# Kernel tuning notes

Hardware: AMD Instinct MI355X
Metric: run time of the kernel (lower is better)

The kernel has to match this reference:

```python
import jax, jax.numpy as jnp
import numpy as np

N = 6000          # num nodes (max_nodes)
E = 192000        # num edges
NTYPES = 100
NCLUST = 4        # hardcoded num_nodes=4 in diff_pool_net.__init__
OUT = 16
BN_EPS = 1e-5

PARAM_SHAPES = {
    'emb_w': (NTYPES, 64),
    # gnn1_pool: GNN(64, 64, 4, lin=True); DenseSAGEConv: lin_rel (no bias) + lin_root (bias)
    'pw1r': (64, 64), 'pw1l': (64, 64), 'pb1': (64,),
    'pw2r': (64, 64), 'pw2l': (64, 64), 'pb2': (64,),
    'pw3r': (NCLUST, 64), 'pw3l': (NCLUST, 64), 'pb3': (NCLUST,),
    'plin_w': (NCLUST, 2 * 64 + NCLUST), 'plin_b': (NCLUST,),
    # gnn1_embed: GNN(64, 64, 64, lin=False)
    'ew1r': (64, 64), 'ew1l': (64, 64), 'eb1': (64,),
    'ew2r': (64, 64), 'ew2l': (64, 64), 'eb2': (64,),
    'ew3r': (64, 64), 'ew3l': (64, 64), 'eb3': (64,),
    'lin1_w': (64, 192), 'lin1_b': (64,),
    'lin2_w': (OUT, 64), 'lin2_b': (OUT,),
    'embl_w': (32, 192), 'embl_b': (32,),
    'lin3_w': (OUT, 32 + OUT), 'lin3_b': (OUT,),
}


def _lin(x, w, b=None):
    y = x @ w.T
    return y if b is None else y + b


def _sage(x, adj, wr, wl, b):
    # DenseSAGEConv: mean-aggregate over dense adj, then lin_rel(agg) + lin_root(x)
    agg = jnp.matmul(adj, x)
    deg = jnp.clip(jnp.sum(adj, axis=-1, keepdims=True), 1.0, None)
    return _lin(agg / deg, wr) + _lin(x, wl, b)


def _bn(x):
    # training-mode BatchNorm1d with default gamma=1, beta=0 (biased variance)
    c = x.shape[-1]
    xf = x.reshape(-1, c)
    m = jnp.mean(xf, axis=0)
    v = jnp.var(xf, axis=0)
    return ((xf - m) * jax.lax.rsqrt(v + BN_EPS)).reshape(x.shape)


def _gnn(x, adj, wr1, wl1, b1, wr2, wl2, b2, wr3, wl3, b3, lw=None, lb=None):
    x1 = _bn(jax.nn.relu(_sage(x, adj, wr1, wl1, b1)))
    x2 = _bn(jax.nn.relu(_sage(x1, adj, wr2, wl2, b2)))
    x3 = _bn(jax.nn.relu(_sage(x2, adj, wr3, wl3, b3)))
    xc = jnp.concatenate([x1, x2, x3], axis=-1)
    if lw is not None:
        xc = jax.nn.relu(_lin(xc, lw, lb))
    return xc


def _forward(p, edge_index, node_types):
    # to_dense_adj: scatter-add edges into a dense [1, N, N] adjacency
    adj = jnp.zeros((N, N), jnp.float32).at[edge_index[0], edge_index[1]].add(1.0)[None]
    x = p['emb_w'][node_types][None]                      # [1, N, 64]
    s = _gnn(x, adj, p['pw1r'], p['pw1l'], p['pb1'],
             p['pw2r'], p['pw2l'], p['pb2'],
             p['pw3r'], p['pw3l'], p['pb3'],
             p['plin_w'], p['plin_b'])                    # [1, N, 4]
    xe = _gnn(x, adj, p['ew1r'], p['ew1l'], p['eb1'],
              p['ew2r'], p['ew2l'], p['eb2'],
              p['ew3r'], p['ew3l'], p['eb3'])             # [1, N, 192]
    x_embed = _lin(xe, p['embl_w'], p['embl_b'])          # [1, N, 32]
    # dense_diff_pool pooled features: softmax(S)^T @ X (pooled adj/losses are unused downstream)
    ssm = jax.nn.softmax(s, axis=-1)
    s_x = jnp.einsum('bnk,bnc->bkc', ssm, xe)             # [1, 4, 192]
    s_x = jax.nn.relu(_lin(s_x, p['lin1_w'], p['lin1_b']))
    s_x = _lin(s_x, p['lin2_w'], p['lin2_b'])             # [1, 4, OUT]
    # one_hot=True branch: per-node gather of its cluster row (vectorized form of the python loop)
    idx = jnp.argmax(s, axis=-1)                          # [1, N]
    res = jnp.take(s_x[0], idx[0], axis=0)[None]          # [1, N, OUT]
    return _lin(jnp.concatenate([x_embed, res], axis=-1), p['lin3_w'], p['lin3_b'])


def setup_inputs() -> dict:
    key = jax.random.key(0)
    ks = jax.random.split(key, len(PARAM_SHAPES) + 2)
    inp = {n: jax.random.normal(k, shp, jnp.float32) * 0.1
           for (n, shp), k in zip(PARAM_SHAPES.items(), ks)}
    inp['edge_index'] = jax.random.randint(ks[-2], (2, E), 0, N)
    inp['node_types'] = jax.random.randint(ks[-1], (N,), 0, NTYPES)
    return inp


def reference(edge_index, node_types, emb_w, pw1r, pw1l, pb1, pw2r, pw2l, pb2,
              pw3r, pw3l, pb3, plin_w, plin_b, ew1r, ew1l, eb1, ew2r, ew2l, eb2,
              ew3r, ew3l, eb3, lin1_w, lin1_b, lin2_w, lin2_b, embl_w, embl_b,
              lin3_w, lin3_b):
    args = locals()
    p = {k: args[k] for k in PARAM_SHAPES}
    return _forward(p, edge_index, node_types)
```

## Files before the change

kernel.cpp:

```cpp
#include <hip/hip_runtime.h>
#include <hip/hip_bf16.h>

#define NN 6000
#define EE 192000

#define W_DEG     0
#define W_CUR     6000
#define W_STATS   12000
#define W_SXACC   12768
#define W_ZEND    13536
#define W_FLAG    13536
#define W_ROWPTR  13540
#define W_COL     19544
#define W_X0      211544
#define W_ZP1     595544
#define W_ZP2     979544
#define W_ZP3     1363544
#define W_ZE1     1387544
#define W_ZE2     1771544
#define W_ZE3     2155544
#define W_S       2539544
#define W_SX2     2563544
#define W_PAR     2563608

struct PtrTab {
  const void* src[29];
  int off[29];
  int cnt[29];
};

__device__ __forceinline__ float bf2f(unsigned short h) {
  return __uint_as_float(((unsigned)h) << 16);
}
__device__ __forceinline__ int rfl(int x) { return __builtin_amdgcn_readfirstlane(x); }

__global__ void k_detect(const void* emb, int* flag) {
  __shared__ int bad;
  if (threadIdx.x == 0) bad = 0;
  __syncthreads();
  const unsigned short* p = (const unsigned short*)emb;
  float v0 = bf2f(p[threadIdx.x]);
  float v1 = bf2f(p[threadIdx.x + 256]);
  if (!(fabsf(v0) <= 100.f) || !(fabsf(v1) <= 100.f)) bad = 1;
  __syncthreads();
  if (threadIdx.x == 0) flag[0] = bad ? 0 : 1;
}

__global__ void k_convert(PtrTab tab, float* base, const int* flag) {
  int b = blockIdx.x;
  const void* s = tab.src[b];
  float* d = base + tab.off[b];
  int n = tab.cnt[b];
  bool bf = (flag[0] == 1);
  if (bf) {
    const unsigned short* sp = (const unsigned short*)s;
    for (int i = threadIdx.x; i < n; i += 256) d[i] = bf2f(sp[i]);
  } else {
    const float* sp = (const float*)s;
    for (int i = threadIdx.x; i < n; i += 256) d[i] = sp[i];
  }
}

__global__ void k_deg(const int* __restrict__ ei, int* __restrict__ deg) {
  int e = blockIdx.x * 256 + threadIdx.x;
  if (e < EE) atomicAdd(&deg[ei[e]], 1);
}

__global__ void k_scan(const int* __restrict__ deg, int* __restrict__ rowptr) {
  __shared__ int part[1024];
  int t = threadIdx.x;
  int base = t * 6;
  int loc[6]; int s = 0;
#pragma unroll
  for (int j = 0; j < 6; ++j) { int i = base + j; int v = (i < NN) ? deg[i] : 0; loc[j] = s; s += v; }
  part[t] = s;
  __syncthreads();
  for (int off = 1; off < 1024; off <<= 1) {
    int v = part[t];
    int add = (t >= off) ? part[t - off] : 0;
    __syncthreads();
    part[t] = v + add;
    __syncthreads();
  }
  int pre = (t == 0) ? 0 : part[t - 1];
#pragma unroll
  for (int j = 0; j < 6; ++j) { int i = base + j; if (i <= NN) rowptr[i] = pre + loc[j]; }
}

__global__ void k_scatter(const int* __restrict__ ei, const int* __restrict__ rowptr,
                          int* __restrict__ cur, int* __restrict__ col) {
  int e = blockIdx.x * 256 + threadIdx.x;
  if (e < EE) {
    int s = ei[e], d = ei[EE + e];
    int pos = atomicAdd(&cur[s], 1);
    col[rowptr[s] + pos] = d;
  }
}

__global__ void k_emb(const float* __restrict__ emb, const int* __restrict__ nt, float* __restrict__ x0) {
  int t = blockIdx.x * 256 + threadIdx.x;
  int i = t >> 4, q = t & 15;
  *(float4*)&x0[i * 64 + q * 4] = *(const float4*)&emb[nt[i] * 64 + q * 4];
}

template <int OUT, bool HS>
__device__ __forceinline__ void sage_body(
    const float* __restrict__ in_z, const float* __restrict__ in_stats,
    const float* __restrict__ wr, const float* __restrict__ wl, const float* __restrict__ bias,
    const int* __restrict__ rowptr, const int* __restrict__ col,
    float* __restrict__ out_z, float* __restrict__ out_stats,
    int vb, int total_waves,
    float* __restrict__ wrT, float* __restrict__ wlT, float* __restrict__ bs,
    float (* __restrict__ vec)[2][64], float (* __restrict__ red)[2][64]) {
  int tid = threadIdx.x, lane = tid & 63, wv = tid >> 6;

  for (int i = tid; i < 64 * OUT; i += 256) {
    int f = i >> 6, k = i & 63;
    wrT[k * (OUT + 1) + f] = wr[i];
    wlT[k * (OUT + 1) + f] = wl[i];
  }
  if (tid < OUT) bs[tid] = bias[tid];

  float m = 0.f, r = 1.f;
  if (HS) {
    float s = in_stats[lane], q = in_stats[64 + lane];
    m = s * (1.f / NN);
    r = rsqrtf(q * (1.f / NN) - m * m + 1e-5f);
  }
  __syncthreads();

  float accs = 0.f, accq = 0.f;
  int ol = lane & (OUT - 1);
  int wave_id = vb * 4 + wv;
  for (int n = wave_id; n < NN; n += total_waves) {
    float x = (in_z[n * 64 + lane] - m) * r;
    int rs = rfl(rowptr[n]), re = rfl(rowptr[n + 1]);
    int cnt = re - rs;
    float sz = 0.f;
    for (int base = rs; base < re; base += 64) {
      int ci = base + lane;
      int colv = col[ci < re ? ci : (re - 1)];
      int full = re - base; if (full > 64) full = 64;
      int ng8 = (full + 7) >> 3;
      for (int g = 0; g < ng8; ++g) {
        int e0 = g * 8;
#pragma unroll
        for (int u = 0; u < 8; ++u) {
          int j = __builtin_amdgcn_readlane(colv, e0 + u);
          float v = in_z[j * 64 + lane];
          sz += (e0 + u < full) ? v : 0.f;
        }
      }
    }
    float fc = (float)cnt;
    float inv = 1.f / (float)(cnt > 0 ? cnt : 1);
    float a = (sz - fc * m) * r * inv;
    vec[wv][0][lane] = a;
    vec[wv][1][lane] = x;
    float y = bs[ol];
    const float* va = &vec[wv][0][0];
    const float* vx = &vec[wv][1][0];
#pragma unroll
    for (int kk = 0; kk < 16; ++kk) {
      const float4 a4 = *(const float4*)(va + kk * 4);
      const float4 x4 = *(const float4*)(vx + kk * 4);
      int k0 = kk * 4;
      y += a4.x * wrT[(k0 + 0) * (OUT + 1) + ol] + x4.x * wlT[(k0 + 0) * (OUT + 1) + ol];
      y += a4.y * wrT[(k0 + 1) * (OUT + 1) + ol] + x4.y * wlT[(k0 + 1) * (OUT + 1) + ol];
      y += a4.z * wrT[(k0 + 2) * (OUT + 1) + ol] + x4.z * wlT[(k0 + 2) * (OUT + 1) + ol];
      y += a4.w * wrT[(k0 + 3) * (OUT + 1) + ol] + x4.w * wlT[(k0 + 3) * (OUT + 1) + ol];
    }
    float z = fmaxf(y, 0.f);
    if (lane < OUT) {
      out_z[n * OUT + lane] = z;
      accs += z; accq += z * z;
    }
  }
  if (lane < OUT) { red[wv][0][lane] = accs; red[wv][1][lane] = accq; }
  __syncthreads();
  if (tid < OUT) {
    float s = red[0][0][tid] + red[1][0][tid] + red[2][0][tid] + red[3][0][tid];
    float q = red[0][1][tid] + red[1][1][tid] + red[2][1][tid] + red[3][1][tid];
    atomicAdd(&out_stats[tid], s);
    atomicAdd(&out_stats[64 + tid], q);
  }
}

template <int OUTA, int OUTB, bool HS>
__global__ __launch_bounds__(256, 4) void k_dual(
    const float* __restrict__ inA, const float* __restrict__ stA,
    const float* __restrict__ wrA, const float* __restrict__ wlA, const float* __restrict__ bA,
    float* __restrict__ outA, float* __restrict__ ostA,
    const float* __restrict__ inB, const float* __restrict__ stB,
    const float* __restrict__ wrB, const float* __restrict__ wlB, const float* __restrict__ bB,
    float* __restrict__ outB, float* __restrict__ ostB,
    const int* __restrict__ rowptr, const int* __restrict__ col, int G) {
  __shared__ float wrT[64 * 65];
  __shared__ float wlT[64 * 65];
  __shared__ float bs[64];
  __shared__ float vec[4][2][64];
  __shared__ float red[4][2][64];
  int bx = (int)blockIdx.x;
  int hi = (bx >> 2) & 1;
  int vb = (bx >> 3) * 4 + (bx & 3);
  if (hi == 0)
    sage_body<OUTA, HS>(inA, stA, wrA, wlA, bA, rowptr, col, outA, ostA,
                        vb, G * 4, wrT, wlT, bs, vec, red);
  else
    sage_body<OUTB, HS>(inB, stB, wrB, wlB, bB, rowptr, col, outB, ostB,
                        vb, G * 4, wrT, wlT, bs, vec, red);
}

__global__ __launch_bounds__(256) void k_pool(
    const float* __restrict__ zp1, const float* __restrict__ zp2, const float* __restrict__ zp3,
    const float* __restrict__ sp1, const float* __restrict__ sp2, const float* __restrict__ sp3,
    const float* __restrict__ ze1, const float* __restrict__ ze2, const float* __restrict__ ze3,
    const float* __restrict__ se1, const float* __restrict__ se2, const float* __restrict__ se3,
    const float* __restrict__ plw, const float* __restrict__ plb,
    float* __restrict__ s_out, float* __restrict__ sx_acc) {
  __shared__ float red[4][12][64];
  int tid = threadIdx.x, lane = tid & 63, wv = tid >> 6;

  float mp1 = sp1[lane] * (1.f / NN); float rp1 = rsqrtf(sp1[64 + lane] * (1.f / NN) - mp1 * mp1 + 1e-5f);
  float mp2 = sp2[lane] * (1.f / NN); float rp2 = rsqrtf(sp2[64 + lane] * (1.f / NN) - mp2 * mp2 + 1e-5f);
  float mp3 = 0.f, rp3 = 1.f;
  if (lane < 4) { mp3 = sp3[lane] * (1.f / NN); rp3 = rsqrtf(sp3[64 + lane] * (1.f / NN) - mp3 * mp3 + 1e-5f); }
  float me1 = se1[lane] * (1.f / NN); float re1 = rsqrtf(se1[64 + lane] * (1.f / NN) - me1 * me1 + 1e-5f);
  float me2 = se2[lane] * (1.f / NN); float re2 = rsqrtf(se2[64 + lane] * (1.f / NN) - me2 * me2 + 1e-5f);
  float me3 = se3[lane] * (1.f / NN); float re3 = rsqrtf(se3[64 + lane] * (1.f / NN) - me3 * me3 + 1e-5f);

  float w0a = plw[0 * 132 + lane], w0b = plw[0 * 132 + 64 + lane], w0c = (lane < 4) ? plw[0 * 132 + 128 + lane] : 0.f;
  float w1a = plw[1 * 132 + lane], w1b = plw[1 * 132 + 64 + lane], w1c = (lane < 4) ? plw[1 * 132 + 128 + lane] : 0.f;
  float w2a = plw[2 * 132 + lane], w2b = plw[2 * 132 + 64 + lane], w2c = (lane < 4) ? plw[2 * 132 + 128 + lane] : 0.f;
  float w3a = plw[3 * 132 + lane], w3b = plw[3 * 132 + 64 + lane], w3c = (lane < 4) ? plw[3 * 132 + 128 + lane] : 0.f;
  float pb0 = plb[0], pb1v = plb[1], pb2v = plb[2], pb3v = plb[3];

  float acc[12];
#pragma unroll
  for (int u = 0; u < 12; ++u) acc[u] = 0.f;

  int wave_id = blockIdx.x * 4 + wv;
  for (int n = wave_id; n < NN; n += 1500) {
    float a = (zp1[n * 64 + lane] - mp1) * rp1;
    float b = (zp2[n * 64 + lane] - mp2) * rp2;
    float c = (lane < 4) ? ((zp3[n * 4 + lane] - mp3) * rp3) : 0.f;
    float p0 = a * w0a + b * w0b + c * w0c;
    float p1 = a * w1a + b * w1b + c * w1c;
    float p2 = a * w2a + b * w2b + c * w2c;
    float p3 = a * w3a + b * w3b + c * w3c;
#pragma unroll
    for (int off = 1; off < 64; off <<= 1) {
      p0 += __shfl_xor(p0, off);
      p1 += __shfl_xor(p1, off);
      p2 += __shfl_xor(p2, off);
      p3 += __shfl_xor(p3, off);
    }
    float s0 = fmaxf(p0 + pb0, 0.f), s1 = fmaxf(p1 + pb1v, 0.f);
    float s2 = fmaxf(p2 + pb2v, 0.f), s3 = fmaxf(p3 + pb3v, 0.f);
    if (lane < 4) {
      float sv = (lane == 0) ? s0 : (lane == 1) ? s1 : (lane == 2) ? s2 : s3;
      s_out[n * 4 + lane] = sv;
    }
    float mx = fmaxf(fmaxf(s0, s1), fmaxf(s2, s3));
    float e0 = __expf(s0 - mx), e1 = __expf(s1 - mx), e2 = __expf(s2 - mx), e3 = __expf(s3 - mx);
    float inv = 1.f / (e0 + e1 + e2 + e3);
    e0 *= inv; e1 *= inv; e2 *= inv; e3 *= inv;
    float x1 = (ze1[n * 64 + lane] - me1) * re1;
    float x2 = (ze2[n * 64 + lane] - me2) * re2;
    float x3 = (ze3[n * 64 + lane] - me3) * re3;
    acc[0] += e0 * x1; acc[1] += e0 * x2; acc[2] += e0 * x3;
    acc[3] += e1 * x1; acc[4] += e1 * x2; acc[5] += e1 * x3;
    acc[6] += e2 * x1; acc[7] += e2 * x2; acc[8] += e2 * x3;
    acc[9] += e3 * x1; acc[10] += e3 * x2; acc[11] += e3 * x3;
  }
#pragma unroll
  for (int u = 0; u < 12; ++u) red[wv][u][lane] = acc[u];
  __syncthreads();
  for (int u = tid; u < 768; u += 256) {
    int f = u & 63, q = u >> 6;
    float v = red[0][q][f] + red[1][q][f] + red[2][q][f] + red[3][q][f];
    int k = q / 3, slot = q - 3 * k;
    atomicAdd(&sx_acc[k * 192 + slot * 64 + f], v);
  }
}

__global__ void k_mlp(const float* __restrict__ sx, const float* __restrict__ l1w, const float* __restrict__ l1b,
                      const float* __restrict__ l2w, const float* __restrict__ l2b, float* __restrict__ sx2) {
  __shared__ float tl[4][64];
  int tid = threadIdx.x;
  int k = tid >> 6, f = tid & 63;
  float v = l1b[f];
  for (int c = 0; c < 192; ++c) v += sx[k * 192 + c] * l1w[f * 192 + c];
  tl[k][f] = fmaxf(v, 0.f);
  __syncthreads();
  if (tid < 64) {
    int kk = tid >> 4, o = tid & 15;
    float u = l2b[o];
#pragma unroll
    for (int j = 0; j < 64; ++j) u += tl[kk][j] * l2w[o * 64 + j];
    sx2[kk * 16 + o] = u;
  }
}

__global__ __launch_bounds__(256) void k_final(
    const float* __restrict__ ze1, const float* __restrict__ ze2, const float* __restrict__ ze3,
    const float* __restrict__ se1, const float* __restrict__ se2, const float* __restrict__ se3,
    const float* __restrict__ ew, const float* __restrict__ ebv,
    const float* __restrict__ l3w, const float* __restrict__ l3b,
    const float* __restrict__ s_out, const float* __restrict__ sx2,
    const int* __restrict__ flag, void* __restrict__ out) {
  __shared__ float ewT[192 * 33];
  __shared__ float l3T[48 * 17];
  __shared__ float ebs[32], l3bs[16];
  __shared__ float xev[4][192];
  __shared__ float xed[4][32];
  int tid = threadIdx.x, lane = tid & 63, wv = tid >> 6;

  for (int i = tid; i < 6144; i += 256) { int cp = i / 192, c = i - cp * 192; ewT[c * 33 + cp] = ew[i]; }
  for (int i = tid; i < 768; i += 256) { int o = i / 48, j = i - o * 48; l3T[j * 17 + o] = l3w[i]; }
  if (tid < 32) ebs[tid] = ebv[tid];
  if (tid < 16) l3bs[tid] = l3b[tid];

  float me1 = se1[lane] * (1.f / NN); float re1 = rsqrtf(se1[64 + lane] * (1.f / NN) - me1 * me1 + 1e-5f);
  float me2 = se2[lane] * (1.f / NN); float re2 = rsqrtf(se2[64 + lane] * (1.f / NN) - me2 * me2 + 1e-5f);
  float me3 = se3[lane] * (1.f / NN); float re3 = rsqrtf(se3[64 + lane] * (1.f / NN) - me3 * me3 + 1e-5f);
  bool bf = (flag[0] == 1);
  __syncthreads();

  int h = lane >> 5, L = lane & 31;
  int wave_id = blockIdx.x * 4 + wv;
  for (int n = wave_id; n < NN; n += 2048) {
    float x1 = (ze1[n * 64 + lane] - me1) * re1;
    float x2 = (ze2[n * 64 + lane] - me2) * re2;
    float x3 = (ze3[n * 64 + lane] - me3) * re3;
    xev[wv][lane] = x1;
    xev[wv][64 + lane] = x2;
    xev[wv][128 + lane] = x3;
    float v = (h == 0) ? ebs[L] : 0.f;
    int cb = h * 96;
#pragma unroll
    for (int c4 = 0; c4 < 24; ++c4) {
      const float4 xv = *(const float4*)&xev[wv][cb + c4 * 4];
      int c0 = cb + c4 * 4;
      v += xv.x * ewT[(c0 + 0) * 33 + L];
      v += xv.y * ewT[(c0 + 1) * 33 + L];
      v += xv.z * ewT[(c0 + 2) * 33 + L];
      v += xv.w * ewT[(c0 + 3) * 33 + L];
    }
    v += __shfl_xor(v, 32);
    if (h == 0) xed[wv][L] = v;
    if (lane < 16) {
      int idx = 0; float best = s_out[n * 4 + 0];
      float c1 = s_out[n * 4 + 1]; if (c1 > best) { best = c1; idx = 1; }
      float c2 = s_out[n * 4 + 2]; if (c2 > best) { best = c2; idx = 2; }
      float c3 = s_out[n * 4 + 3]; if (c3 > best) { best = c3; idx = 3; }
      float racc = l3bs[lane];
#pragma unroll
      for (int j = 0; j < 32; ++j) racc += xed[wv][j] * l3T[j * 17 + lane];
      const float* sxr = sx2 + idx * 16;
#pragma unroll
      for (int j = 0; j < 16; ++j) racc += sxr[j] * l3T[(32 + j) * 17 + lane];
      if (bf) ((__hip_bfloat16*)out)[n * 16 + lane] = __float2bfloat16(racc);
      else    ((float*)out)[n * 16 + lane] = racc;
    }
  }
}

extern "C" void kernel_launch(void* const* d_in, const int* in_sizes, int n_in,
                              void* d_out, int out_size, void* d_ws, size_t ws_size,
                              hipStream_t stream) {
  float* F = (float*)d_ws;
  int* I = (int*)d_ws;

  static const int pcnt[29] = {6400, 4096, 4096, 64, 4096, 4096, 64, 256, 256, 4, 528, 4,
                               4096, 4096, 64, 4096, 4096, 64, 4096, 4096, 64,
                               12288, 64, 1024, 16, 6144, 32, 768, 16};
  int poff[29];
  { int a = 0; for (int i = 0; i < 29; ++i) { poff[i] = a; a += pcnt[i]; } }

  PtrTab tab;
  for (int i = 0; i < 29; ++i) { tab.src[i] = d_in[i]; tab.off[i] = poff[i]; tab.cnt[i] = pcnt[i]; }

  const int* ei = (const int*)d_in[29];
  const int* nt = (const int*)d_in[30];

  int* deg = I + W_DEG;
  int* cur = I + W_CUR;
  int* rowptr = I + W_ROWPTR;
  int* col = I + W_COL;
  int* flag = I + W_FLAG;
  float* st = F + W_STATS;
  float* sxacc = F + W_SXACC;
  float* x0 = F + W_X0;
  float* zp1 = F + W_ZP1; float* zp2 = F + W_ZP2; float* zp3 = F + W_ZP3;
  float* ze1 = F + W_ZE1; float* ze2 = F + W_ZE2; float* ze3 = F + W_ZE3;
  float* sbuf = F + W_S;
  float* sx2 = F + W_SX2;
  float* P = F + W_PAR;
#define PP(i) (P + poff[i])

  hipMemsetAsync(d_ws, 0, (size_t)W_ZEND * 4, stream);
  k_detect<<<1, 256, 0, stream>>>(d_in[0], flag);
  k_convert<<<29, 256, 0, stream>>>(tab, P, flag);
  k_deg<<<750, 256, 0, stream>>>(ei, deg);
  k_scan<<<1, 1024, 0, stream>>>(deg, rowptr);
  k_scatter<<<750, 256, 0, stream>>>(ei, rowptr, cur, col);
  k_emb<<<375, 256, 0, stream>>>(PP(0), nt, x0);

  k_dual<64, 64, false><<<1024, 256, 0, stream>>>(
      x0, nullptr, PP(1), PP(2), PP(3), zp1, st + 0 * 128,
      x0, nullptr, PP(12), PP(13), PP(14), ze1, st + 3 * 128,
      rowptr, col, 512);
  k_dual<64, 64, true><<<1024, 256, 0, stream>>>(
      zp1, st + 0 * 128, PP(4), PP(5), PP(6), zp2, st + 1 * 128,
      ze1, st + 3 * 128, PP(15), PP(16), PP(17), ze2, st + 4 * 128,
      rowptr, col, 512);
  k_dual<4, 64, true><<<1024, 256, 0, stream>>>(
      zp2, st + 1 * 128, PP(7), PP(8), PP(9), zp3, st + 2 * 128,
      ze2, st + 4 * 128, PP(18), PP(19), PP(20), ze3, st + 5 * 128,
      rowptr, col, 512);

  k_pool<<<375, 256, 0, stream>>>(zp1, zp2, zp3, st + 0 * 128, st + 1 * 128, st + 2 * 128,
                                  ze1, ze2, ze3, st + 3 * 128, st + 4 * 128, st + 5 * 128,
                                  PP(10), PP(11), sbuf, sxacc);
  k_mlp<<<1, 256, 0, stream>>>(sxacc, PP(21), PP(22), PP(23), PP(24), sx2);
  k_final<<<512, 256, 0, stream>>>(ze1, ze2, ze3, st + 3 * 128, st + 4 * 128, st + 5 * 128,
                                   PP(25), PP(26), PP(27), PP(28), sbuf, sx2, flag, d_out);
}
```

Measured before the change: 291.6 us.

## Fuse prelude kernels, fold MLP into final, use 1024-thread SAGE blocks

```diff
diff --git a/kernel.cpp b/kernel.cpp
--- a/kernel.cpp
+++ b/kernel.cpp
@@ -34,36 +34,50 @@
 }
 __device__ __forceinline__ int rfl(int x) { return __builtin_amdgcn_readfirstlane(x); }
 
-__global__ void k_detect(const void* emb, int* flag) {
-  __shared__ int bad;
-  if (threadIdx.x == 0) bad = 0;
-  __syncthreads();
-  const unsigned short* p = (const unsigned short*)emb;
-  float v0 = bf2f(p[threadIdx.x]);
-  float v1 = bf2f(p[threadIdx.x + 256]);
-  if (!(fabsf(v0) <= 100.f) || !(fabsf(v1) <= 100.f)) bad = 1;
-  __syncthreads();
-  if (threadIdx.x == 0) flag[0] = bad ? 0 : 1;
-}
-
-__global__ void k_convert(PtrTab tab, float* base, const int* flag) {
+__global__ __launch_bounds__(256) void k_prelude(
+    PtrTab tab, float* __restrict__ base,
+    const int* __restrict__ nt, float* __restrict__ x0,
+    const int* __restrict__ ei, int* __restrict__ deg, int* __restrict__ flag) {
+  __shared__ int s_ok;
+  int tid = threadIdx.x;
+  const unsigned short* ep = (const unsigned short*)tab.src[0];
+  if (tid == 0) s_ok = 1;
+  __syncthreads();
+  float v0 = bf2f(ep[tid]), v1 = bf2f(ep[tid + 256]);
+  if (!(fabsf(v0) <= 100.f) || !(fabsf(v1) <= 100.f)) atomicAnd(&s_ok, 0);
+  __syncthreads();
+  bool bf = (s_ok != 0);
   int b = blockIdx.x;
-  const void* s = tab.src[b];
-  float* d = base + tab.off[b];
-  int n = tab.cnt[b];
-  bool bf = (flag[0] == 1);
-  if (bf) {
-    const unsigned short* sp = (const unsigned short*)s;
-    for (int i = threadIdx.x; i < n; i += 256) d[i] = bf2f(sp[i]);
+  if (b == 0 && tid == 0) flag[0] = bf ? 1 : 0;
+
+  if (b < 29) {
+    const void* s = tab.src[b];
+    float* d = base + tab.off[b];
+    int n = tab.cnt[b];
+    if (bf) {
+      const unsigned short* sp = (const unsigned short*)s;
+      for (int i = tid; i < n; i += 256) d[i] = bf2f(sp[i]);
+    } else {
+      const float* sp = (const float*)s;
+      for (int i = tid; i < n; i += 256) d[i] = sp[i];
+    }
+  } else if (b < 404) {
+    int t = (b - 29) * 256 + tid;
+    int i = t >> 4, q = t & 15;
+    int row = nt[i];
+    if (bf) {
+      const unsigned short* sp = (const unsigned short*)tab.src[0] + row * 64 + q * 4;
+      float4 o;
+      o.x = bf2f(sp[0]); o.y = bf2f(sp[1]); o.z = bf2f(sp[2]); o.w = bf2f(sp[3]);
+      *(float4*)&x0[i * 64 + q * 4] = o;
+    } else {
+      *(float4*)&x0[i * 64 + q * 4] =
+          *(const float4*)((const float*)tab.src[0] + row * 64 + q * 4);
+    }
   } else {
-    const float* sp = (const float*)s;
-    for (int i = threadIdx.x; i < n; i += 256) d[i] = sp[i];
-  }
-}
-
-__global__ void k_deg(const int* __restrict__ ei, int* __restrict__ deg) {
-  int e = blockIdx.x * 256 + threadIdx.x;
-  if (e < EE) atomicAdd(&deg[ei[e]], 1);
+    int e = (b - 404) * 256 + tid;
+    if (e < EE) atomicAdd(&deg[ei[e]], 1);
+  }
 }
 
 __global__ void k_scan(const int* __restrict__ deg, int* __restrict__ rowptr) {
@@ -95,12 +109,6 @@
     int pos = atomicAdd(&cur[s], 1);
     col[rowptr[s] + pos] = d;
   }
-}
-
-__global__ void k_emb(const float* __restrict__ emb, const int* __restrict__ nt, float* __restrict__ x0) {
-  int t = blockIdx.x * 256 + threadIdx.x;
-  int i = t >> 4, q = t & 15;
-  *(float4*)&x0[i * 64 + q * 4] = *(const float4*)&emb[nt[i] * 64 + q * 4];
 }
 
 template <int OUT, bool HS>
@@ -114,7 +122,7 @@
     float (* __restrict__ vec)[2][64], float (* __restrict__ red)[2][64]) {
   int tid = threadIdx.x, lane = tid & 63, wv = tid >> 6;
 
-  for (int i = tid; i < 64 * OUT; i += 256) {
+  for (int i = tid; i < 64 * OUT; i += 1024) {
     int f = i >> 6, k = i & 63;
     wrT[k * (OUT + 1) + f] = wr[i];
     wlT[k * (OUT + 1) + f] = wl[i];
@@ -131,7 +139,7 @@
 
   float accs = 0.f, accq = 0.f;
   int ol = lane & (OUT - 1);
-  int wave_id = vb * 4 + wv;
+  int wave_id = vb * 16 + wv;
   for (int n = wave_id; n < NN; n += total_waves) {
     float x = (in_z[n * 64 + lane] - m) * r;
     int rs = rfl(rowptr[n]), re = rfl(rowptr[n + 1]);
@@ -172,22 +180,23 @@
     }
     float z = fmaxf(y, 0.f);
     if (lane < OUT) {
-      out_z[n * OUT + lane] = z;
+      __builtin_nontemporal_store(z, &out_z[n * OUT + lane]);
       accs += z; accq += z * z;
     }
   }
   if (lane < OUT) { red[wv][0][lane] = accs; red[wv][1][lane] = accq; }
   __syncthreads();
   if (tid < OUT) {
-    float s = red[0][0][tid] + red[1][0][tid] + red[2][0][tid] + red[3][0][tid];
-    float q = red[0][1][tid] + red[1][1][tid] + red[2][1][tid] + red[3][1][tid];
+    float s = 0.f, q = 0.f;
+#pragma unroll
+    for (int w = 0; w < 16; ++w) { s += red[w][0][tid]; q += red[w][1][tid]; }
     atomicAdd(&out_stats[tid], s);
     atomicAdd(&out_stats[64 + tid], q);
   }
 }
 
 template <int OUTA, int OUTB, bool HS>
-__global__ __launch_bounds__(256, 4) void k_dual(
+__global__ __launch_bounds__(1024, 8) void k_dual(
     const float* __restrict__ inA, const float* __restrict__ stA,
     const float* __restrict__ wrA, const float* __restrict__ wlA, const float* __restrict__ bA,
     float* __restrict__ outA, float* __restrict__ ostA,
@@ -198,17 +207,17 @@
   __shared__ float wrT[64 * 65];
   __shared__ float wlT[64 * 65];
   __shared__ float bs[64];
-  __shared__ float vec[4][2][64];
-  __shared__ float red[4][2][64];
+  __shared__ float vec[16][2][64];
+  __shared__ float red[16][2][64];
   int bx = (int)blockIdx.x;
   int hi = (bx >> 2) & 1;
   int vb = (bx >> 3) * 4 + (bx & 3);
   if (hi == 0)
     sage_body<OUTA, HS>(inA, stA, wrA, wlA, bA, rowptr, col, outA, ostA,
-                        vb, G * 4, wrT, wlT, bs, vec, red);
+                        vb, G * 16, wrT, wlT, bs, vec, red);
   else
     sage_body<OUTB, HS>(inB, stB, wrB, wlB, bB, rowptr, col, outB, ostB,
-                        vb, G * 4, wrT, wlT, bs, vec, red);
+                        vb, G * 16, wrT, wlT, bs, vec, red);
 }
 
 __global__ __launch_bounds__(256) void k_pool(
@@ -284,42 +293,50 @@
   }
 }
 
-__global__ void k_mlp(const float* __restrict__ sx, const float* __restrict__ l1w, const float* __restrict__ l1b,
-                      const float* __restrict__ l2w, const float* __restrict__ l2b, float* __restrict__ sx2) {
-  __shared__ float tl[4][64];
-  int tid = threadIdx.x;
-  int k = tid >> 6, f = tid & 63;
-  float v = l1b[f];
-  for (int c = 0; c < 192; ++c) v += sx[k * 192 + c] * l1w[f * 192 + c];
-  tl[k][f] = fmaxf(v, 0.f);
-  __syncthreads();
-  if (tid < 64) {
-    int kk = tid >> 4, o = tid & 15;
-    float u = l2b[o];
-#pragma unroll
-    for (int j = 0; j < 64; ++j) u += tl[kk][j] * l2w[o * 64 + j];
-    sx2[kk * 16 + o] = u;
-  }
-}
-
 __global__ __launch_bounds__(256) void k_final(
     const float* __restrict__ ze1, const float* __restrict__ ze2, const float* __restrict__ ze3,
     const float* __restrict__ se1, const float* __restrict__ se2, const float* __restrict__ se3,
     const float* __restrict__ ew, const float* __restrict__ ebv,
     const float* __restrict__ l3w, const float* __restrict__ l3b,
-    const float* __restrict__ s_out, const float* __restrict__ sx2,
+    const float* __restrict__ s_out,
+    const float* __restrict__ sxacc,
+    const float* __restrict__ l1w, const float* __restrict__ l1b,
+    const float* __restrict__ l2w, const float* __restrict__ l2b,
     const int* __restrict__ flag, void* __restrict__ out) {
   __shared__ float ewT[192 * 33];
   __shared__ float l3T[48 * 17];
   __shared__ float ebs[32], l3bs[16];
   __shared__ float xev[4][192];
   __shared__ float xed[4][32];
+  __shared__ float tl[4][64];
+  __shared__ float sx2l[64];
   int tid = threadIdx.x, lane = tid & 63, wv = tid >> 6;
 
   for (int i = tid; i < 6144; i += 256) { int cp = i / 192, c = i - cp * 192; ewT[c * 33 + cp] = ew[i]; }
   for (int i = tid; i < 768; i += 256) { int o = i / 48, j = i - o * 48; l3T[j * 17 + o] = l3w[i]; }
   if (tid < 32) ebs[tid] = ebv[tid];
   if (tid < 16) l3bs[tid] = l3b[tid];
+
+  {
+    int k = tid >> 6, f = tid & 63;
+    float v = l1b[f];
+    const float4* Ar = (const float4*)(sxacc + k * 192);
+    const float4* Wr = (const float4*)(l1w + f * 192);
+#pragma unroll 8
+    for (int c4 = 0; c4 < 48; ++c4) {
+      float4 a = Ar[c4], w = Wr[c4];
+      v += a.x * w.x + a.y * w.y + a.z * w.z + a.w * w.w;
+    }
+    tl[k][f] = fmaxf(v, 0.f);
+  }
+  __syncthreads();
+  if (tid < 64) {
+    int kk = tid >> 4, o = tid & 15;
+    float u = l2b[o];
+#pragma unroll
+    for (int j = 0; j < 64; ++j) u += tl[kk][j] * l2w[o * 64 + j];
+    sx2l[kk * 16 + o] = u;
+  }
 
   float me1 = se1[lane] * (1.f / NN); float re1 = rsqrtf(se1[64 + lane] * (1.f / NN) - me1 * me1 + 1e-5f);
   float me2 = se2[lane] * (1.f / NN); float re2 = rsqrtf(se2[64 + lane] * (1.f / NN) - me2 * me2 + 1e-5f);
@@ -357,7 +374,7 @@
       float racc = l3bs[lane];
 #pragma unroll
       for (int j = 0; j < 32; ++j) racc += xed[wv][j] * l3T[j * 17 + lane];
-      const float* sxr = sx2 + idx * 16;
+      const float* sxr = sx2l + idx * 16;
 #pragma unroll
       for (int j = 0; j < 16; ++j) racc += sxr[j] * l3T[(32 + j) * 17 + lane];
       if (bf) ((__hip_bfloat16*)out)[n * 16 + lane] = __float2bfloat16(racc);
@@ -395,35 +412,31 @@
   float* zp1 = F + W_ZP1; float* zp2 = F + W_ZP2; float* zp3 = F + W_ZP3;
   float* ze1 = F + W_ZE1; float* ze2 = F + W_ZE2; float* ze3 = F + W_ZE3;
   float* sbuf = F + W_S;
-  float* sx2 = F + W_SX2;
   float* P = F + W_PAR;
 #define PP(i) (P + poff[i])
 
   hipMemsetAsync(d_ws, 0, (size_t)W_ZEND * 4, stream);
-  k_detect<<<1, 256, 0, stream>>>(d_in[0], flag);
-  k_convert<<<29, 256, 0, stream>>>(tab, P, flag);
-  k_deg<<<750, 256, 0, stream>>>(ei, deg);
+  k_prelude<<<1154, 256, 0, stream>>>(tab, P, nt, x0, ei, deg, flag);
   k_scan<<<1, 1024, 0, stream>>>(deg, rowptr);
   k_scatter<<<750, 256, 0, stream>>>(ei, rowptr, cur, col);
-  k_emb<<<375, 256, 0, stream>>>(PP(0), nt, x0);
-
-  k_dual<64, 64, false><<<1024, 256, 0, stream>>>(
+
+  k_dual<64, 64, false><<<512, 1024, 0, stream>>>(
       x0, nullptr, PP(1), PP(2), PP(3), zp1, st + 0 * 128,
       x0, nullptr, PP(12), PP(13), PP(14), ze1, st + 3 * 128,
-      rowptr, col, 512);
-  k_dual<64, 64, true><<<1024, 256, 0, stream>>>(
+      rowptr, col, 256);
+  k_dual<64, 64, true><<<512, 1024, 0, stream>>>(
       zp1, st + 0 * 128, PP(4), PP(5), PP(6), zp2, st + 1 * 128,
       ze1, st + 3 * 128, PP(15), PP(16), PP(17), ze2, st + 4 * 128,
-      rowptr, col, 512);
-  k_dual<4, 64, true><<<1024, 256, 0, stream>>>(
+      rowptr, col, 256);
+  k_dual<4, 64, true><<<512, 1024, 0, stream>>>(
       zp2, st + 1 * 128, PP(7), PP(8), PP(9), zp3, st + 2 * 128,
       ze2, st + 4 * 128, PP(18), PP(19), PP(20), ze3, st + 5 * 128,
-      rowptr, col, 512);
+      rowptr, col, 256);
 
   k_pool<<<375, 256, 0, stream>>>(zp1, zp2, zp3, st + 0 * 128, st + 1 * 128, st + 2 * 128,
                                   ze1, ze2, ze3, st + 3 * 128, st + 4 * 128, st + 5 * 128,
                                   PP(10), PP(11), sbuf, sxacc);
-  k_mlp<<<1, 256, 0, stream>>>(sxacc, PP(21), PP(22), PP(23), PP(24), sx2);
   k_final<<<512, 256, 0, stream>>>(ze1, ze2, ze3, st + 3 * 128, st + 4 * 128, st + 5 * 128,
-                                   PP(25), PP(26), PP(27), PP(28), sbuf, sx2, flag, d_out);
-}
+                                   PP(25), PP(26), PP(27), PP(28), sbuf,
+                                   sxacc, PP(21), PP(22), PP(23), PP(24), flag, d_out);
+}
```

Result: slower. 431.6 us (+48.0%).
